# Kernel tuning notes

Hardware: AMD Instinct MI355X
Metric: run time of the kernel (lower is better)

## Reference

```python
import jax, jax.numpy as jnp
import numpy as np


def fwht(x):
    """Fast Walsh-Hadamard transform over the last dim (power of 2), normalized by 1/sqrt(n)."""
    n = x.shape[-1]
    orig_shape = x.shape
    x = x.reshape(-1, n)
    h = 1
    while h < n:
        x = x.reshape(-1, n // (2 * h), 2, h)
        a = x[:, :, 0, :]
        b = x[:, :, 1, :]
        x = jnp.stack([a + b, a - b], axis=2)
        h *= 2
    x = x.reshape(orig_shape)
    return x * (1.0 / jnp.sqrt(jnp.asarray(n, dtype=x.dtype)))


def act_quant(x, bits):
    """Per-token absmax symmetric quantization with straight-through estimator."""
    qb = 2.0 ** (bits - 1) - 1.0  # 127 for 8 bits
    scale = qb / jnp.clip(jnp.max(jnp.abs(x), axis=-1, keepdims=True), 1e-5, None)
    q = jnp.clip(jnp.round(x * scale), -qb, qb) / scale
    return x + jax.lax.stop_gradient(q - x)


def weight_quant(w):
    """BitNet b1.58 ternary weight quantization (per-tensor mean-abs scale) with STE."""
    scale = jnp.clip(jnp.mean(jnp.abs(w)), 1e-5, None)
    q = jnp.clip(jnp.round(w / scale), -1.0, 1.0) * scale
    return w + jax.lax.stop_gradient(q - w)


def hbitlinear(x, w, bits):
    # Hadamard rotate activations, quantize acts + ternary weights, then GEMM.
    xh = fwht(x)
    xq = act_quant(xh, bits)
    wq = weight_quant(w)
    return jnp.einsum('bsh,oh->bso', xq, wq)


def setup_inputs() -> dict:
    key = jax.random.key(0)
    k1, k2, k3 = jax.random.split(key, 3)
    B, S, H = 4, 2048, 2048
    I = 4096  # intermediate = hidden * mlp_ratio(2.0)
    hidden_states = jax.random.normal(k1, (B, S, H), dtype=jnp.float32)
    w_up = jax.random.normal(k2, (I, H), dtype=jnp.float32) * 0.02
    w_down = jax.random.normal(k3, (H, I), dtype=jnp.float32) * 0.02
    return {"hidden_states": hidden_states, "w_up": w_up, "w_down": w_down}


def reference(hidden_states, w_up, w_down):
    ACT_BITS = 8
    h = hbitlinear(hidden_states, w_up, ACT_BITS)   # (B, S, I)
    h = jnp.square(jax.nn.relu(h))                  # ReLU^2
    # dropout with p=0.0 (eval/identity)
    out = hbitlinear(h, w_down, ACT_BITS)           # (B, S, H)
    return out
```

## Files before the change

kernel.cpp:

```cpp
#include <hip/hip_runtime.h>
#include <hip/hip_bf16.h>

typedef int i32x4 __attribute__((ext_vector_type(4)));

#define GLL16(g, l) __builtin_amdgcn_global_load_lds( \
    (const __attribute__((address_space(1))) void*)(g), \
    (__attribute__((address_space(3))) void*)(l), 16, 0, 0)

#define CFENCE() asm volatile("" ::: "memory")

__global__ __launch_bounds__(256) void abs_sum_kernel(const float* __restrict__ w, int n4,
                                                      double* __restrict__ out)
{
    double acc = 0.0;
    const float4* w4 = (const float4*)w;
    for (int i = blockIdx.x * blockDim.x + threadIdx.x; i < n4; i += gridDim.x * blockDim.x) {
        float4 v = w4[i];
        acc += (double)fabsf(v.x) + (double)fabsf(v.y) + (double)fabsf(v.z) + (double)fabsf(v.w);
    }
    for (int o = 32; o > 0; o >>= 1) acc += __shfl_down(acc, o, 64);
    __shared__ double part[4];
    int lane = threadIdx.x & 63, wv = threadIdx.x >> 6;
    if (lane == 0) part[wv] = acc;
    __syncthreads();
    if (threadIdx.x == 0) atomicAdd(out, part[0] + part[1] + part[2] + part[3]);
}

__global__ __launch_bounds__(256) void wquant_kernel(const float* __restrict__ w, int n4,
                                                     const double* __restrict__ sum, double inv_count,
                                                     char* __restrict__ out)
{
    float s = (float)(sum[0] * inv_count);
    s = fmaxf(s, 1e-5f);
    const float4* w4 = (const float4*)w;
    char4* o4 = (char4*)out;
    for (int i = blockIdx.x * blockDim.x + threadIdx.x; i < n4; i += gridDim.x * blockDim.x) {
        float4 v = w4[i];
        char4 c;
        c.x = (char)fminf(fmaxf(rintf(v.x / s), -1.0f), 1.0f);
        c.y = (char)fminf(fmaxf(rintf(v.y / s), -1.0f), 1.0f);
        c.z = (char)fminf(fmaxf(rintf(v.z / s), -1.0f), 1.0f);
        c.w = (char)fminf(fmaxf(rintf(v.w / s), -1.0f), 1.0f);
        o4[i] = c;
    }
}

template<int NS>
__device__ __forceinline__ void hreg(float* v)
{
    #pragma unroll
    for (int h = 1; h < (1 << NS); h <<= 1)
        #pragma unroll
        for (int i = 0; i < 16; i++)
            if ((i & h) == 0) { float a = v[i], b = v[i + h]; v[i] = a + b; v[i + h] = a - b; }
}

template<int N, int TOKS>
__global__ __launch_bounds__(256) void fwht_quant_kernel(
    const float* __restrict__ in, long in_stride,
    char* __restrict__ outq, long out_stride,
    float* __restrict__ scales)
{
    constexpr int L = 256 / TOKS;
    static_assert(N == 16 * L, "N must be 16*threads-per-token");
    __shared__ float sx[TOKS * N];
    __shared__ float red[4];

    const int tid = threadIdx.x;
    const int tk  = tid / L;
    const int lt  = tid % L;
    const long tok = (long)blockIdx.x * TOKS + tk;
    const float* row = in + tok * in_stride;
    float* s = sx + tk * N;

    float v[16];
    {
        const float4* r4 = (const float4*)(row + (size_t)lt * 16);
        float4 a[4];
        #pragma unroll
        for (int i = 0; i < 4; i++) a[i] = r4[i];
        #pragma unroll
        for (int i = 0; i < 4; i++) {
            v[4*i] = a[i].x; v[4*i+1] = a[i].y; v[4*i+2] = a[i].z; v[4*i+3] = a[i].w;
        }
    }
    hreg<4>(v);
    #pragma unroll
    for (int i = 0; i < 4; i++)
        *(float4*)(s + lt * 16 + 4 * i) = make_float4(v[4*i], v[4*i+1], v[4*i+2], v[4*i+3]);
    __syncthreads();

    const int o = lt & 15, ss = lt >> 4;
    #pragma unroll
    for (int j = 0; j < 16; j++) v[j] = s[o + 256 * ss + 16 * j];
    hreg<(L == 256) ? 4 : 3>(v);
    #pragma unroll
    for (int j = 0; j < 16; j++) s[o + 256 * ss + 16 * j] = v[j];
    __syncthreads();

    #pragma unroll
    for (int j = 0; j < 16; j++) v[j] = s[o + 16 * ss + L * j];
    hreg<4>(v);

    const float rn = 1.0f / sqrtf((float)N);
    float m = 0.0f;
    #pragma unroll
    for (int j = 0; j < 16; j++) { v[j] *= rn; m = fmaxf(m, fabsf(v[j])); }
    for (int off = 32; off > 0; off >>= 1) m = fmaxf(m, __shfl_down(m, off, 64));
    if ((tid & 63) == 0) red[tid >> 6] = m;
    __syncthreads();
    float mm;
    if (TOKS == 1) mm = fmaxf(fmaxf(red[0], red[1]), fmaxf(red[2], red[3]));
    else           mm = fmaxf(red[2 * tk], red[2 * tk + 1]);
    mm = fmaxf(mm, 1e-5f);
    const float sc = 127.0f / mm;
    if (lt == 0) scales[tok] = sc;
    __syncthreads();

    char* ct = (char*)sx + tk * N;
    #pragma unroll
    for (int j = 0; j < 16; j++) {
        float q = fminf(fmaxf(rintf(v[j] * sc), -127.0f), 127.0f);
        ct[o + 16 * ss + L * j] = (char)q;
    }
    __syncthreads();
    int4* dst = (int4*)(outq + tok * out_stride);
    dst[lt] = ((const int4*)ct)[lt];
}

#define BM2 256
#define BN2 256
#define BK2 64

__global__ __launch_bounds__(512, 2) void gemm_bt_kernel(
    const char* __restrict__ A, int lda,
    const char* __restrict__ B, int ldb,
    float* __restrict__ C, int ldc,
    int K, int lognx,
    const float* __restrict__ sx,
    const double* __restrict__ wsum, double inv_count,
    int do_relu2)
{
    __shared__ __align__(16) char As[4][BM2 * BK2];
    __shared__ __align__(16) char Bs[4][BN2 * BK2];

    const int bid = blockIdx.x;
    const int xcd = bid & 7;
    const int n = bid >> 3;
    const int nper = gridDim.x >> 3;
    const int bx = n & ((1 << lognx) - 1);
    const int by = xcd * (nper >> lognx) + (n >> lognx);
    const int row0 = by * BM2;
    const int col0 = bx * BN2;

    const int tid = threadIdx.x;
    const int lane = tid & 63;
    const int w = tid >> 6;
    const int wr = w >> 2;
    const int wc = w & 3;

    i32x4 acc[8][4] = {};

    const int srow = w * 16 + (lane >> 2);
    const int sseg = ((lane & 3) ^ ((lane >> 3) & 3)) << 4;
    const char* Ag0 = A + (size_t)(row0 + srow) * lda + sseg;
    const char* Ag1 = Ag0 + (size_t)128 * lda;
    const char* Bg0 = B + (size_t)(col0 + srow) * ldb + sseg;
    const char* Bg1 = Bg0 + (size_t)128 * ldb;
    const int wdst = w * 1024;

    const int fr = lane & 15;
    const int fks = lane >> 4;
    const int rsw = ((fks ^ ((fr >> 1) & 3)) << 4);
    const int aoff = (wr * 128 + fr) * BK2 + rsw;
    const int boff = (wc * 64  + fr) * BK2 + rsw;

    const int NT = K >> 6;

    auto stage = [&](int tt) {
        const int sb = tt & 3;
        const int ko = tt * BK2;
        GLL16(Ag0 + ko, &As[sb][wdst]);
        GLL16(Ag1 + ko, &As[sb][wdst + 8192]);
        GLL16(Bg0 + ko, &Bs[sb][wdst]);
        GLL16(Bg1 + ko, &Bs[sb][wdst + 8192]);
    };
    auto compute = [&](int cb) {
        const char* as = As[cb];
        const char* bs = Bs[cb];
        i32x4 af[8], bf[4];
        #pragma unroll
        for (int i = 0; i < 8; ++i) af[i] = *(const i32x4*)(as + aoff + i * 1024);
        #pragma unroll
        for (int j = 0; j < 4; ++j) bf[j] = *(const i32x4*)(bs + boff + j * 1024);
        __builtin_amdgcn_s_setprio(1);
        #pragma unroll
        for (int i = 0; i < 8; ++i)
            #pragma unroll
            for (int j = 0; j < 4; ++j)
                acc[i][j] = __builtin_amdgcn_mfma_i32_16x16x64_i8(af[i], bf[j], acc[i][j], 0, 0, 0);
        __builtin_amdgcn_s_setprio(0);
    };

    stage(0); stage(1); stage(2);
    asm volatile("s_waitcnt vmcnt(8)" ::: "memory");
    __builtin_amdgcn_s_barrier();
    CFENCE();

    int t = 0;
    for (; t < NT - 3; ++t) {
        stage(t + 3);
        compute(t & 3);
        asm volatile("s_waitcnt vmcnt(8)" ::: "memory");
        __builtin_amdgcn_s_barrier();
        CFENCE();
    }
    compute(t & 3);
    asm volatile("s_waitcnt vmcnt(4)" ::: "memory");
    __builtin_amdgcn_s_barrier();
    CFENCE();
    ++t;
    compute(t & 3);
    asm volatile("s_waitcnt vmcnt(0)" ::: "memory");
    __builtin_amdgcn_s_barrier();
    CFENCE();
    ++t;
    compute(t & 3);

    float sw = (float)(wsum[0] * inv_count);
    sw = fmaxf(sw, 1e-5f);
    const int qd = lane >> 4;
    #pragma unroll
    for (int i = 0; i < 8; ++i) {
        #pragma unroll
        for (int r = 0; r < 4; ++r) {
            int rowm = row0 + wr * 128 + i * 16 + qd * 4 + r;
            float esc = sw / sx[rowm];
            float* crow = C + (size_t)rowm * ldc + col0 + wc * 64;
            #pragma unroll
            for (int j = 0; j < 4; ++j) {
                float v = (float)acc[i][j][r] * esc;
                if (do_relu2) { v = fmaxf(v, 0.0f); v = v * v; }
                crow[j * 16 + fr] = v;
            }
        }
    }
}

extern "C" void kernel_launch(void* const* d_in, const int* in_sizes, int n_in,
                              void* d_out, int out_size, void* d_ws, size_t ws_size,
                              hipStream_t stream)
{
    const float* X   = (const float*)d_in[0];
    const float* Wup = (const float*)d_in[1];
    const float* Wdn = (const float*)d_in[2];
    float* out = (float*)d_out;

    const int Mtok = 8192, H = 2048, I = 4096;
    const int NW = H * I;

    char* ws = (char*)d_ws;
    double* sums = (double*)ws;
    float* sx1 = (float*)(ws + 1024);
    float* sx2 = (float*)(ws + 1024 + 32768);
    char* wqup = ws + (1 << 20);
    char* wqdn = wqup + (size_t)NW;
    char* xq1  = wqdn + (size_t)NW;
    float* hbuf = (float*)(xq1 + (size_t)Mtok * H);

    hipMemsetAsync(sums, 0, 16, stream);
    abs_sum_kernel<<<512, 256, 0, stream>>>(Wup, NW / 4, &sums[0]);
    abs_sum_kernel<<<512, 256, 0, stream>>>(Wdn, NW / 4, &sums[1]);
    const double invc = 1.0 / (double)NW;
    wquant_kernel<<<1024, 256, 0, stream>>>(Wup, NW / 4, &sums[0], invc, wqup);
    wquant_kernel<<<1024, 256, 0, stream>>>(Wdn, NW / 4, &sums[1], invc, wqdn);

    fwht_quant_kernel<2048, 2><<<Mtok / 2, 256, 0, stream>>>(X, H, xq1, H, sx1);
    gemm_bt_kernel<<<(I / BN2) * (Mtok / BM2), 512, 0, stream>>>(
        xq1, H, wqup, H, hbuf, I, H, 4, sx1, &sums[0], invc, 1);
    fwht_quant_kernel<4096, 1><<<Mtok, 256, 0, stream>>>(hbuf, I, (char*)hbuf, 4 * I, sx2);
    gemm_bt_kernel<<<(H / BN2) * (Mtok / BM2), 512, 0, stream>>>(
        (const char*)hbuf, 4 * I, wqdn, I, out, H, I, 3, sx2, &sums[1], invc, 0);
}
```

Before: 405.8 us.

## Split int8 GEMM tile into two half-phases interleaving A/B global loads with MFMA

Restructures the main int8 MFMA loop so each K-tile is processed in two halves: the first four A fragments plus the B fragments are read and the A prefetch is issued, then the second A half is read and the B prefetch is issued, with barriers between phases. This spreads the global-to-LDS loads across the compute and shrinks the live A fragment registers from 8 to 4, aiming for better overlap and lower register pressure. It adds three extra workgroup barriers per tile, which may add sync stalls.

```diff
diff --git a/kernel.cpp b/kernel.cpp
--- a/kernel.cpp
+++ b/kernel.cpp
@@ -177,55 +177,74 @@
 
     const int NT = K >> 6;
 
-    auto stage = [&](int tt) {
+    auto stageA = [&](int tt) {
         const int sb = tt & 3;
         const int ko = tt * BK2;
         GLL16(Ag0 + ko, &As[sb][wdst]);
         GLL16(Ag1 + ko, &As[sb][wdst + 8192]);
+    };
+    auto stageB = [&](int tt) {
+        const int sb = tt & 3;
+        const int ko = tt * BK2;
         GLL16(Bg0 + ko, &Bs[sb][wdst]);
         GLL16(Bg1 + ko, &Bs[sb][wdst + 8192]);
     };
-    auto compute = [&](int cb) {
+
+    auto tile_body = [&](int t, bool do_stage) __attribute__((always_inline)) {
+        const int cb = t & 3;
         const char* as = As[cb];
         const char* bs = Bs[cb];
-        i32x4 af[8], bf[4];
-        #pragma unroll
-        for (int i = 0; i < 8; ++i) af[i] = *(const i32x4*)(as + aoff + i * 1024);
+        i32x4 af[4], bf[4], af2[4];
+        #pragma unroll
+        for (int i = 0; i < 4; ++i) af[i] = *(const i32x4*)(as + aoff + i * 1024);
         #pragma unroll
         for (int j = 0; j < 4; ++j) bf[j] = *(const i32x4*)(bs + boff + j * 1024);
+        if (do_stage) stageA(t + 3);
+        __builtin_amdgcn_s_barrier();
+        CFENCE();
         __builtin_amdgcn_s_setprio(1);
         #pragma unroll
-        for (int i = 0; i < 8; ++i)
+        for (int i = 0; i < 4; ++i)
             #pragma unroll
             for (int j = 0; j < 4; ++j)
                 acc[i][j] = __builtin_amdgcn_mfma_i32_16x16x64_i8(af[i], bf[j], acc[i][j], 0, 0, 0);
         __builtin_amdgcn_s_setprio(0);
+        __builtin_amdgcn_s_barrier();
+        CFENCE();
+        #pragma unroll
+        for (int i = 0; i < 4; ++i) af2[i] = *(const i32x4*)(as + aoff + (4 + i) * 1024);
+        if (do_stage) stageB(t + 3);
+        __builtin_amdgcn_s_barrier();
+        CFENCE();
+        __builtin_amdgcn_s_setprio(1);
+        #pragma unroll
+        for (int i = 0; i < 4; ++i)
+            #pragma unroll
+            for (int j = 0; j < 4; ++j)
+                acc[4 + i][j] = __builtin_amdgcn_mfma_i32_16x16x64_i8(af2[i], bf[j], acc[4 + i][j], 0, 0, 0);
+        __builtin_amdgcn_s_setprio(0);
     };
 
-    stage(0); stage(1); stage(2);
+    stageA(0); stageB(0); stageA(1); stageB(1); stageA(2); stageB(2);
     asm volatile("s_waitcnt vmcnt(8)" ::: "memory");
     __builtin_amdgcn_s_barrier();
     CFENCE();
 
-    int t = 0;
-    for (; t < NT - 3; ++t) {
-        stage(t + 3);
-        compute(t & 3);
+    for (int t = 0; t <= NT - 4; ++t) {
+        tile_body(t, true);
         asm volatile("s_waitcnt vmcnt(8)" ::: "memory");
         __builtin_amdgcn_s_barrier();
         CFENCE();
     }
-    compute(t & 3);
+    tile_body(NT - 3, false);
     asm volatile("s_waitcnt vmcnt(4)" ::: "memory");
     __builtin_amdgcn_s_barrier();
     CFENCE();
-    ++t;
-    compute(t & 3);
+    tile_body(NT - 2, false);
     asm volatile("s_waitcnt vmcnt(0)" ::: "memory");
     __builtin_amdgcn_s_barrier();
     CFENCE();
-    ++t;
-    compute(t & 3);
+    tile_body(NT - 1, false);
 
     float sw = (float)(wsum[0] * inv_count);
     sw = fmaxf(sw, 1e-5f);
```

New measurement: 399.8 us. Within noise of the previous version (-1.5%).

## Use 32x32x32 int8 MFMA tiles in GEMM and swizzle FWHT loads through LDS

Applied to the files above, without the earlier changes.

The int8 GEMM inner loop switches from 16x16x64 MFMA instructions to 32x32x32 ones. This reorganises the accumulator layout, the LDS fragment addressing and the epilogue row mapping, and it halves the number of fragment loads per k-step. The FWHT kernel now reads rows with coalesced strided float4 loads and stages them through swizzled shared memory before the per-thread transform, where before each thread read a contiguous 64-byte chunk. This trades an extra LDS round trip and barrier for better global coalescing and a higher-throughput MFMA shape.

```diff
diff --git a/kernel.cpp b/kernel.cpp
--- a/kernel.cpp
+++ b/kernel.cpp
@@ -1,7 +1,8 @@
 #include <hip/hip_runtime.h>
 #include <hip/hip_bf16.h>
 
-typedef int i32x4 __attribute__((ext_vector_type(4)));
+typedef int i32x4  __attribute__((ext_vector_type(4)));
+typedef int i32x16 __attribute__((ext_vector_type(16)));
 
 #define GLL16(g, l) __builtin_amdgcn_global_load_lds( \
     (const __attribute__((address_space(1))) void*)(g), \
@@ -73,15 +74,30 @@
     const float* row = in + tok * in_stride;
     float* s = sx + tk * N;
 
+    float4 a[4];
+    {
+        const float4* r4 = (const float4*)row;
+        #pragma unroll
+        for (int i = 0; i < 4; i++) a[i] = r4[lt + L * i];
+    }
+    {
+        const int c  = lt & 3;
+        const int pc = (c ^ ((lt >> 3) & 3)) << 2;
+        #pragma unroll
+        for (int i = 0; i < 4; i++) {
+            const int r64 = (lt >> 2) + (L >> 2) * i;
+            *(float4*)(s + r64 * 16 + pc) = a[i];
+        }
+    }
+    __syncthreads();
+
     float v[16];
     {
-        const float4* r4 = (const float4*)(row + (size_t)lt * 16);
-        float4 a[4];
-        #pragma unroll
-        for (int i = 0; i < 4; i++) a[i] = r4[i];
-        #pragma unroll
-        for (int i = 0; i < 4; i++) {
-            v[4*i] = a[i].x; v[4*i+1] = a[i].y; v[4*i+2] = a[i].z; v[4*i+3] = a[i].w;
+        const int sw = (lt >> 1) & 3;
+        #pragma unroll
+        for (int c = 0; c < 4; c++) {
+            float4 t = *(const float4*)(s + lt * 16 + ((c ^ sw) << 2));
+            v[4*c] = t.x; v[4*c+1] = t.y; v[4*c+2] = t.z; v[4*c+3] = t.w;
         }
     }
     hreg<4>(v);
@@ -159,7 +175,7 @@
     const int wr = w >> 2;
     const int wc = w & 3;
 
-    i32x4 acc[8][4] = {};
+    i32x16 acc[4][2] = {};
 
     const int srow = w * 16 + (lane >> 2);
     const int sseg = ((lane & 3) ^ ((lane >> 3) & 3)) << 4;
@@ -169,11 +185,11 @@
     const char* Bg1 = Bg0 + (size_t)128 * ldb;
     const int wdst = w * 1024;
 
-    const int fr = lane & 15;
-    const int fks = lane >> 4;
-    const int rsw = ((fks ^ ((fr >> 1) & 3)) << 4);
-    const int aoff = (wr * 128 + fr) * BK2 + rsw;
-    const int boff = (wc * 64  + fr) * BK2 + rsw;
+    const int r31 = lane & 31;
+    const int ksel = lane >> 5;
+    const int fsw = (r31 >> 1) & 3;
+    const int abase = (wr * 128 + r31) * BK2;
+    const int bbase = (wc * 64  + r31) * BK2;
 
     const int NT = K >> 6;
 
@@ -185,20 +201,29 @@
         GLL16(Bg0 + ko, &Bs[sb][wdst]);
         GLL16(Bg1 + ko, &Bs[sb][wdst + 8192]);
     };
-    auto compute = [&](int cb) {
+    auto compute = [&](int t) __attribute__((always_inline)) {
+        const int cb = t & 3;
         const char* as = As[cb];
         const char* bs = Bs[cb];
-        i32x4 af[8], bf[4];
-        #pragma unroll
-        for (int i = 0; i < 8; ++i) af[i] = *(const i32x4*)(as + aoff + i * 1024);
-        #pragma unroll
-        for (int j = 0; j < 4; ++j) bf[j] = *(const i32x4*)(bs + boff + j * 1024);
+        i32x4 af[4][2], bf[2][2];
+        #pragma unroll
+        for (int i = 0; i < 4; ++i)
+            #pragma unroll
+            for (int p = 0; p < 2; ++p)
+                af[i][p] = *(const i32x4*)(as + abase + i * 32 * BK2 + (((2 * p + ksel) ^ fsw) << 4));
+        #pragma unroll
+        for (int j = 0; j < 2; ++j)
+            #pragma unroll
+            for (int p = 0; p < 2; ++p)
+                bf[j][p] = *(const i32x4*)(bs + bbase + j * 32 * BK2 + (((2 * p + ksel) ^ fsw) << 4));
         __builtin_amdgcn_s_setprio(1);
         #pragma unroll
-        for (int i = 0; i < 8; ++i)
+        for (int p = 0; p < 2; ++p)
             #pragma unroll
-            for (int j = 0; j < 4; ++j)
-                acc[i][j] = __builtin_amdgcn_mfma_i32_16x16x64_i8(af[i], bf[j], acc[i][j], 0, 0, 0);
+            for (int i = 0; i < 4; ++i)
+                #pragma unroll
+                for (int j = 0; j < 2; ++j)
+                    acc[i][j] = __builtin_amdgcn_mfma_i32_32x32x32_i8(af[i][p], bf[j][p], acc[i][j], 0, 0, 0);
         __builtin_amdgcn_s_setprio(0);
     };
 
@@ -207,41 +232,37 @@
     __builtin_amdgcn_s_barrier();
     CFENCE();
 
-    int t = 0;
-    for (; t < NT - 3; ++t) {
+    for (int t = 0; t <= NT - 4; ++t) {
         stage(t + 3);
-        compute(t & 3);
+        compute(t);
         asm volatile("s_waitcnt vmcnt(8)" ::: "memory");
         __builtin_amdgcn_s_barrier();
         CFENCE();
     }
-    compute(t & 3);
+    compute(NT - 3);
     asm volatile("s_waitcnt vmcnt(4)" ::: "memory");
     __builtin_amdgcn_s_barrier();
     CFENCE();
-    ++t;
-    compute(t & 3);
+    compute(NT - 2);
     asm volatile("s_waitcnt vmcnt(0)" ::: "memory");
     __builtin_amdgcn_s_barrier();
     CFENCE();
-    ++t;
-    compute(t & 3);
+    compute(NT - 1);
 
     float sw = (float)(wsum[0] * inv_count);
     sw = fmaxf(sw, 1e-5f);
-    const int qd = lane >> 4;
-    #pragma unroll
-    for (int i = 0; i < 8; ++i) {
-        #pragma unroll
-        for (int r = 0; r < 4; ++r) {
-            int rowm = row0 + wr * 128 + i * 16 + qd * 4 + r;
-            float esc = sw / sx[rowm];
-            float* crow = C + (size_t)rowm * ldc + col0 + wc * 64;
+    #pragma unroll
+    for (int i = 0; i < 4; ++i) {
+        #pragma unroll
+        for (int reg = 0; reg < 16; ++reg) {
+            const int rowm = row0 + wr * 128 + i * 32 + (reg & 3) + 8 * (reg >> 2) + 4 * ksel;
+            const float esc = sw / sx[rowm];
+            float* crow = C + (size_t)rowm * ldc + col0 + wc * 64 + r31;
             #pragma unroll
-            for (int j = 0; j < 4; ++j) {
-                float v = (float)acc[i][j][r] * esc;
+            for (int j = 0; j < 2; ++j) {
+                float v = (float)acc[i][j][reg] * esc;
                 if (do_relu2) { v = fmaxf(v, 0.0f); v = v * v; }
-                crow[j * 16 + fr] = v;
+                crow[j * 32] = v;
             }
         }
     }
```

Result: slower. 415.6 us (+2.4%).
